# Kernel tuning notes

Hardware: AMD Instinct MI355X
Metric: run time of the kernel (lower is better)

## Reference

```python
import jax, jax.numpy as jnp
import numpy as np

RATIOS = (2, 2, 2)
IN_SIZE = 512
DATA_SIZE = 2
NOISE_BANDS = 5
TARGET_SIZE = int(np.prod(RATIOS))  # 8


def conv1d(x, w, b, stride):
    # cc.get_padding(3, stride, mode='centered'): total pad = 3 - stride = 1 -> (left, right) = (0, 1)
    y = jax.lax.conv_general_dilated(
        x, w, window_strides=(stride,), padding=[(0, 1)],
        dimension_numbers=('NCH', 'OIH', 'NCH'))
    return y + b[None, :, None]


def mod_sigmoid(x):
    return 2.0 * jax.nn.sigmoid(x) ** 2.3 + 1e-7


def amp_to_impulse_response(amp, target_size):
    # amp: [..., noise_bands] real, treated as complex spectrum with zero imag
    ir = jnp.fft.irfft(amp)                      # [..., 2*(nb-1)]
    fs = ir.shape[-1]
    ir = jnp.roll(ir, fs // 2, axis=-1)
    n = jnp.arange(fs, dtype=ir.dtype)
    win = 0.5 * (1.0 - jnp.cos(2.0 * jnp.pi * n / fs))  # periodic hann (torch default)
    ir = ir * win
    pad = int(target_size) - fs                   # 0 for our config
    ir = jnp.pad(ir, [(0, 0)] * (ir.ndim - 1) + [(0, pad)])
    return jnp.roll(ir, -(fs // 2), axis=-1)


def fft_convolve(signal, kernel):
    n = signal.shape[-1]
    pad_cfg = [(0, 0)] * (signal.ndim - 1)
    s = jnp.pad(signal, pad_cfg + [(0, n)])
    k = jnp.pad(kernel, pad_cfg + [(n, 0)])
    out = jnp.fft.irfft(jnp.fft.rfft(s) * jnp.fft.rfft(k))
    return out[..., out.shape[-1] // 2:]


def setup_inputs() -> dict:
    key = jax.random.key(0)
    ks = jax.random.split(key, 8)
    B, T = 16, 4096
    c_out = DATA_SIZE * NOISE_BANDS
    x = jax.random.normal(ks[0], (B, IN_SIZE, T), dtype=jnp.float32)
    noise = jax.random.uniform(ks[1], (B, T // TARGET_SIZE, DATA_SIZE, TARGET_SIZE), dtype=jnp.float32)
    w1 = jax.random.normal(ks[2], (IN_SIZE, IN_SIZE, 3), dtype=jnp.float32) * 0.03
    b1 = jnp.zeros((IN_SIZE,), dtype=jnp.float32)
    w2 = jax.random.normal(ks[3], (IN_SIZE, IN_SIZE, 3), dtype=jnp.float32) * 0.03
    b2 = jnp.zeros((IN_SIZE,), dtype=jnp.float32)
    w3 = jax.random.normal(ks[4], (c_out, IN_SIZE, 3), dtype=jnp.float32) * 0.03
    b3 = jnp.zeros((c_out,), dtype=jnp.float32)
    return {"x": x, "noise": noise, "w1": w1, "b1": b1, "w2": w2, "b2": b2, "w3": w3, "b3": b3}


def reference(x, noise, w1, b1, w2, b2, w3, b3):
    h = conv1d(x, w1, b1, RATIOS[0])
    h = jax.nn.leaky_relu(h, 0.2)
    h = conv1d(h, w2, b2, RATIOS[1])
    h = jax.nn.leaky_relu(h, 0.2)
    h = conv1d(h, w3, b3, RATIOS[2])            # [B, data_size*nb, T']
    amp = mod_sigmoid(h - 5.0)
    amp = jnp.transpose(amp, (0, 2, 1))          # [B, T', data_size*nb]
    B, Tp = amp.shape[0], amp.shape[1]
    amp = amp.reshape(B, Tp, DATA_SIZE, -1)      # [B, T', data_size, nb]
    ir = amp_to_impulse_response(amp, TARGET_SIZE)  # [B, T', data_size, target]
    nz = noise * 2.0 - 1.0                        # torch.rand_like(ir)*2-1
    out = fft_convolve(nz, ir)                    # [B, T', data_size, target]
    out = jnp.transpose(out, (0, 2, 1, 3))        # [B, data_size, T', target]
    return out.reshape(B, DATA_SIZE, -1)          # [B, data_size, T'*target]
```

## Files before the change

kernel.cpp:

```cpp
#include <hip/hip_runtime.h>
#include <math.h>


typedef __attribute__((ext_vector_type(8)))  short bf16x8;
typedef __attribute__((ext_vector_type(16))) float f32x16;

__device__ __forceinline__ unsigned short f2bf_rne(float f) {
    unsigned int u = __float_as_uint(f);
    unsigned int r = u + 0x7fff + ((u >> 16) & 1);
    return (unsigned short)(r >> 16);
}
__device__ __forceinline__ float bf2f(unsigned short h) {
    return __uint_as_float(((unsigned int)h) << 16);
}
__device__ __forceinline__ void gload_lds16(const void* g, void* l) {
    __builtin_amdgcn_global_load_lds(
        (const __attribute__((address_space(1))) unsigned int*)g,
        (__attribute__((address_space(3))) unsigned int*)l, 16, 0, 0);
}
__device__ __forceinline__ int swz1(int r) {
    return ((r >> 1) ^ (r >> 4)) & 7;
}

__global__ void prep_all(const float* __restrict__ W1, const float* __restrict__ W2,
                         short* __restrict__ Wf1, short* __restrict__ Wf2,
                         char* __restrict__ h1p, char* __restrict__ h2t)
{
    const int bid = blockIdx.x;
    const int tid = threadIdx.x;
    if (bid < 1536) {
        const float* W = (bid < 768) ? W1 : W2;
        short* Wf = (bid < 768) ? Wf1 : Wf2;
        int gid = ((bid < 768) ? bid : bid - 768) * 256 + tid;
        int f = gid >> 6, l = gid & 63;
        int ks = f & 1, hl = (f >> 1) & 1;
        int k  = (f >> 2) % 3;
        int rem = (f >> 2) / 3;
        int cob = rem & 15, cb = rem >> 4;
        int co  = cob * 32 + (l & 31);
        int ci0 = cb * 32 + ks * 16 + (l >> 5) * 8;
        bf16x8 o;
#pragma unroll
        for (int j = 0; j < 8; ++j) {
            float v = W[((size_t)co * 512 + ci0 + j) * 3 + k];
            unsigned short hi = f2bf_rne(v);
            o[j] = hl ? (short)f2bf_rne(v - bf2f(hi)) : (short)hi;
        }
        *(bf16x8*)((char*)Wf + (size_t)f * 1024 + l * 16) = o;
    } else {
        int id = (bid - 1536) * 256 + tid;
        if (id < 16384) {
            int b = id >> 10, w = id & 1023;
            *(float*)(h1p + ((size_t)b * 2080 + 2048) * 2048 + (size_t)w * 4) = 0.f;
        } else {
            int id2 = id - 16384;
            int b = id2 >> 10, w = id2 & 1023;
            *(float*)(h2t + ((size_t)b * 1026 + 1024) * 2048 + (size_t)w * 4) = 0.f;
        }
    }
}

__global__ __launch_bounds__(256, 2) void conv1_fused(
    const float* __restrict__ X, const short* __restrict__ Wf,
    const float* __restrict__ Bias, char* __restrict__ Out)
{
    __shared__ char AB[2][16512];

    const int tid = threadIdx.x;
    const int l   = tid & 63;
    const int wid = tid >> 6;
    const int tl0 = l & 31;
    const int lh  = l >> 5;

    int p = blockIdx.x;
    int chunk = p >> 5, slot = p & 31;
    int gl = slot & 15, c = slot >> 4;
    int g = chunk * 16 + gl;
    int zb = g >> 5, y = g & 31;

    const int bt0 = y * 64;
    const int r0  = 2 * bt0;
    const float* Xb = X + (size_t)zb * 512 * 4096;

    const int rg   = tid & 15;
    const int cip  = tid >> 4;
    const int ci   = 2 * cip;
    const int u_hi = ci >> 3;
    const int u_lo = 4 + u_hi;
    const int coff = (ci & 7) * 2;

    f32x16 acc[2][2];
#pragma unroll
    for (int tp = 0; tp < 2; ++tp)
#pragma unroll
        for (int cp = 0; cp < 2; ++cp) acc[tp][cp] = (f32x16)(0.0f);

    const int cbase = c * 8 + wid * 2;

    float4 fx0, fx1, fx2, fx3;
    float  fextra = 0.f;

    auto issue_loads = [&](int cb) {
        const float* s0 = Xb + (size_t)(cb * 32 + 2 * cip) * 4096 + r0 + rg * 8;
        fx0 = *(const float4*)(s0);
        fx1 = *(const float4*)(s0 + 4);
        fx2 = *(const float4*)(s0 + 4096);
        fx3 = *(const float4*)(s0 + 4100);
        if (tid < 32) {
            int rr = r0 + 128;
            fextra = (rr < 4096) ? Xb[(size_t)(cb * 32 + tid) * 4096 + rr] : 0.f;
        }
    };

    auto write_k = [&](char* buf, int k, float a, float b) {
        int r  = rg * 8 + k;
        int sw = swz1(r);
        unsigned int ua = __float_as_uint(a);
        unsigned int ub = __float_as_uint(b);
        float ha = __uint_as_float(ua & 0xffff0000u);
        float hb = __uint_as_float(ub & 0xffff0000u);
        unsigned short la = f2bf_rne(a - ha);
        unsigned short lb = f2bf_rne(b - hb);
        *(unsigned int*)(buf + r * 128 + ((u_hi ^ sw) << 4) + coff) =
            (ua >> 16) | (ub & 0xffff0000u);
        *(unsigned int*)(buf + r * 128 + ((u_lo ^ sw) << 4) + coff) =
            (unsigned int)la | ((unsigned int)lb << 16);
    };
    auto write_lo = [&](char* buf) {
        write_k(buf, 0, fx0.x, fx2.x);
        write_k(buf, 1, fx0.y, fx2.y);
        write_k(buf, 2, fx0.z, fx2.z);
        write_k(buf, 3, fx0.w, fx2.w);
    };
    auto write_hi = [&](char* buf) {
        write_k(buf, 4, fx1.x, fx3.x);
        write_k(buf, 5, fx1.y, fx3.y);
        write_k(buf, 6, fx1.z, fx3.z);
        write_k(buf, 7, fx1.w, fx3.w);
        if (tid < 32) {
            int sw = swz1(128);
            unsigned int ue = __float_as_uint(fextra);
            float he = __uint_as_float(ue & 0xffff0000u);
            unsigned short lo = f2bf_rne(fextra - he);
            int uh = (tid >> 3) ^ sw;
            int ul = (4 + (tid >> 3)) ^ sw;
            *(unsigned short*)(buf + 128 * 128 + (uh << 4) + (tid & 7) * 2) =
                (unsigned short)(ue >> 16);
            *(unsigned short*)(buf + 128 * 128 + (ul << 4) + (tid & 7) * 2) = lo;
        }
    };

    auto wptr = [&](int cb_, int cp, int tap, int ks, int hl) -> const char* {
        size_t f0 = ((((size_t)(cb_ * 16 + cbase + cp) * 3 + tap) * 2 + hl) * 2 + ks);
        return (const char*)Wf + f0 * 1024 + (size_t)l * 16;
    };

    issue_loads(0);
    write_lo(AB[0]);
    write_hi(AB[0]);
    __syncthreads();

    for (int cb = 0; cb < 16; ++cb) {
        const char* Ab = AB[cb & 1];
        char* Wb = (char*)AB[(cb + 1) & 1];

        bf16x8 bbA[12];
#pragma unroll
        for (int ph = 0; ph < 3; ++ph)
#pragma unroll
            for (int cp = 0; cp < 2; ++cp)
#pragma unroll
                for (int hl = 0; hl < 2; ++hl)
                    bbA[ph * 4 + cp * 2 + hl] =
                        *(const bf16x8*)wptr(cb, cp, ph >> 1, ph & 1, hl);
        if (cb < 15) issue_loads(cb + 1);

        __builtin_amdgcn_s_setprio(1);
#pragma unroll
        for (int ph = 0; ph < 3; ++ph) {
            const int tap = ph >> 1, ks = ph & 1;
            bf16x8 a0[2], a1[2];
#pragma unroll
            for (int tp = 0; tp < 2; ++tp) {
                int rl = 2 * (tp * 32 + tl0) + tap;
                int sw = swz1(rl);
                int qb = ks * 2 + lh;
                a0[tp] = *(const bf16x8*)(Ab + rl * 128 + ((qb ^ sw) << 4));
                a1[tp] = *(const bf16x8*)(Ab + rl * 128 + (((qb + 4) ^ sw) << 4));
            }
#pragma unroll
            for (int tp = 0; tp < 2; ++tp)
#pragma unroll
                for (int cp = 0; cp < 2; ++cp) {
                    acc[tp][cp] = __builtin_amdgcn_mfma_f32_32x32x16_bf16(
                        a0[tp], bbA[ph * 4 + cp * 2 + 0], acc[tp][cp], 0, 0, 0);
                    acc[tp][cp] = __builtin_amdgcn_mfma_f32_32x32x16_bf16(
                        a0[tp], bbA[ph * 4 + cp * 2 + 1], acc[tp][cp], 0, 0, 0);
                    acc[tp][cp] = __builtin_amdgcn_mfma_f32_32x32x16_bf16(
                        a1[tp], bbA[ph * 4 + cp * 2 + 0], acc[tp][cp], 0, 0, 0);
                }
        }
        __builtin_amdgcn_s_setprio(0);

        bf16x8 bbB[12];
#pragma unroll
        for (int ph = 3; ph < 6; ++ph)
#pragma unroll
            for (int cp = 0; cp < 2; ++cp)
#pragma unroll
                for (int hl = 0; hl < 2; ++hl)
                    bbB[(ph - 3) * 4 + cp * 2 + hl] =
                        *(const bf16x8*)wptr(cb, cp, ph >> 1, ph & 1, hl);

        if (cb < 15) write_lo(Wb);

        __builtin_amdgcn_s_setprio(1);
#pragma unroll
        for (int ph = 3; ph < 6; ++ph) {
            const int tap = ph >> 1, ks = ph & 1;
            bf16x8 a0[2], a1[2];
#pragma unroll
            for (int tp = 0; tp < 2; ++tp) {
                int rl = 2 * (tp * 32 + tl0) + tap;
                int sw = swz1(rl);
                int qb = ks * 2 + lh;
                a0[tp] = *(const bf16x8*)(Ab + rl * 128 + ((qb ^ sw) << 4));
                a1[tp] = *(const bf16x8*)(Ab + rl * 128 + (((qb + 4) ^ sw) << 4));
            }
#pragma unroll
            for (int tp = 0; tp < 2; ++tp)
#pragma unroll
                for (int cp = 0; cp < 2; ++cp) {
                    acc[tp][cp] = __builtin_amdgcn_mfma_f32_32x32x16_bf16(
                        a0[tp], bbB[(ph - 3) * 4 + cp * 2 + 0], acc[tp][cp], 0, 0, 0);
                    acc[tp][cp] = __builtin_amdgcn_mfma_f32_32x32x16_bf16(
                        a0[tp], bbB[(ph - 3) * 4 + cp * 2 + 1], acc[tp][cp], 0, 0, 0);
                    acc[tp][cp] = __builtin_amdgcn_mfma_f32_32x32x16_bf16(
                        a1[tp], bbB[(ph - 3) * 4 + cp * 2 + 0], acc[tp][cp], 0, 0, 0);
                }
        }
        __builtin_amdgcn_s_setprio(0);

        if (cb < 15) write_hi(Wb);
        __syncthreads();
    }

    const size_t outB = (size_t)zb * 2080 * 2048;
    const int colb = c * 256 + wid * 64 + tl0;
#pragma unroll
    for (int cp = 0; cp < 2; ++cp) {
        int co = colb + cp * 32;
        float bv = Bias[co];
#pragma unroll
        for (int tp = 0; tp < 2; ++tp) {
            int trow = bt0 + tp * 32 + 4 * lh;
#pragma unroll
            for (int r = 0; r < 16; ++r) {
                int row = trow + (r & 3) + 8 * (r >> 2);
                float v = acc[tp][cp][r] + bv;
                v = v < 0.f ? 0.2f * v : v;
                char* po = Out + outB + (size_t)row * 2048;
                unsigned int uv = __float_as_uint(v);
                float hf = __uint_as_float(uv & 0xffff0000u);
                *(unsigned short*)(po + co * 2) = (unsigned short)(uv >> 16);
                *(unsigned short*)(po + 1024 + co * 2) = f2bf_rne(v - hf);
            }
        }
    }
}

#define CONV_UNITS 1032

__global__ __launch_bounds__(256, 2) void conv_mfma(
    const char* __restrict__ Xp, const short* __restrict__ Wf,
    const float* __restrict__ Bias, char* __restrict__ Out,
    int rowsX, int rowsO, int Yt, int mode)
{
    __shared__ char AB[2][16512];

    const int tid = threadIdx.x;
    const int l   = tid & 63;
    const int wid = tid >> 6;
    const int tl0 = l & 31;
    const int lh  = l >> 5;

    int p = blockIdx.x;
    int chunk = p >> 5, slot = p & 31;
    int gl = slot & 15, c = slot >> 4;
    int g = chunk * 16 + gl;
    int zb = g / Yt, y = g - zb * Yt;

    const int bt0 = y * 64;
    const int r0  = 2 * bt0;
    const char* Xb = Xp + (size_t)zb * (size_t)rowsX * 2048;

    f32x16 acc[2][2];
#pragma unroll
    for (int tp = 0; tp < 2; ++tp)
#pragma unroll
        for (int cp = 0; cp < 2; ++cp) acc[tp][cp] = (f32x16)(0.0f);

    const int cbase = c * 8 + wid * 2;

    auto stage = [&](char* buf, int cb) {
#pragma unroll
        for (int i = 0; i < 5; ++i) {
            int u = i * 256 + tid;
            if (u < CONV_UNITS) {
                int r = u >> 3, ul = u & 7;
                int us = ul ^ ((r >> 1) & 7);
                const char* gp = Xb + (size_t)(r0 + r) * 2048
                               + (us >> 2) * 1024 + cb * 64 + (us & 3) * 16;
                gload_lds16(gp, buf + ((size_t)(i * 256 + wid * 64)) * 16);
            }
        }
    };

    stage(AB[0], 0);
    __syncthreads();

    for (int cb = 0; cb < 16; ++cb) {
        if (cb < 15) stage(AB[(cb + 1) & 1], cb + 1);
        const char* Ab = AB[cb & 1];
#pragma unroll
        for (int ph = 0; ph < 6; ++ph) {
            const int tap = ph >> 1, ks = ph & 1;
            bf16x8 a[2][2], bb[2][2];
#pragma unroll
            for (int tp = 0; tp < 2; ++tp) {
                int rl = 2 * (tp * 32 + tl0) + tap;
                int sw = (rl >> 1) & 7;
                int qb = ks * 2 + lh;
                a[0][tp] = *(const bf16x8*)(Ab + rl * 128 + ((qb ^ sw) << 4));
                a[1][tp] = *(const bf16x8*)(Ab + rl * 128 + (((qb + 4) ^ sw) << 4));
            }
#pragma unroll
            for (int cp = 0; cp < 2; ++cp) {
                size_t f0 = ((((size_t)(cb * 16 + cbase + cp) * 3 + tap) * 2 + 0) * 2 + ks);
                const char* wp = (const char*)Wf + f0 * 1024 + l * 16;
                bb[0][cp] = *(const bf16x8*)(wp);
                bb[1][cp] = *(const bf16x8*)(wp + 2048);
            }
#pragma unroll
            for (int tp = 0; tp < 2; ++tp)
#pragma unroll
                for (int cp = 0; cp < 2; ++cp) {
                    acc[tp][cp] = __builtin_amdgcn_mfma_f32_32x32x16_bf16(
                        a[0][tp], bb[0][cp], acc[tp][cp], 0, 0, 0);
                    acc[tp][cp] = __builtin_amdgcn_mfma_f32_32x32x16_bf16(
                        a[0][tp], bb[1][cp], acc[tp][cp], 0, 0, 0);
                    acc[tp][cp] = __builtin_amdgcn_mfma_f32_32x32x16_bf16(
                        a[1][tp], bb[0][cp], acc[tp][cp], 0, 0, 0);
                }
        }
        __syncthreads();
    }

    const size_t outB = (size_t)zb * (size_t)rowsO * 2048;
    const int colb = c * 256 + wid * 64 + tl0;
#pragma unroll
    for (int cp = 0; cp < 2; ++cp) {
        int co = colb + cp * 32;
        float bv = Bias[co];
#pragma unroll
        for (int tp = 0; tp < 2; ++tp) {
            int trow = bt0 + tp * 32 + 4 * lh;
#pragma unroll
            for (int r = 0; r < 16; ++r) {
                int row = trow + (r & 3) + 8 * (r >> 2);
                float v = acc[tp][cp][r] + bv;
                v = v < 0.f ? 0.2f * v : v;
                char* po = Out + outB + (size_t)row * 2048;
                if (mode == 0) {
                    unsigned short hi = f2bf_rne(v);
                    unsigned short lo = f2bf_rne(v - bf2f(hi));
                    *(unsigned short*)(po + co * 2) = hi;
                    *(unsigned short*)(po + 1024 + co * 2) = lo;
                } else {
                    *(float*)(po + (size_t)co * 4) = v;
                }
            }
        }
    }
}

__global__ __launch_bounds__(256) void conv3_tmaj(
    const float* __restrict__ H2, const float* __restrict__ W3,
    const float* __restrict__ B3, const float* __restrict__ Noise,
    float* __restrict__ Out)
{
    __shared__ float W3s[1536][10];
    __shared__ float Xe[32][40];
    __shared__ float Xo[32][40];
    __shared__ float hs[32][12];

    const int b   = blockIdx.y;
    const int t0  = blockIdx.x * 32;
    const int tid = threadIdx.x;
    const int t   = tid & 31;
    const int gch = tid >> 5;

    for (int idx = tid; idx < 15360; idx += 256) {
        int co = idx / 1536;
        int r  = idx - co * 1536;
        W3s[r][co] = W3[idx];
    }

    float acc3[2] = {0.f, 0.f};
    const float* Hb = H2 + (size_t)b * 1026 * 512;

    for (int c0 = 0; c0 < 512; c0 += 32) {
        __syncthreads();
        for (int idx = tid; idx < 33 * 32; idx += 256) {
            int pp = idx >> 5, ci = idx & 31;
            Xe[ci][pp] = Hb[(size_t)(2 * t0 + 2 * pp) * 512 + c0 + ci];
            Xo[ci][pp] = Hb[(size_t)(2 * t0 + 2 * pp + 1) * 512 + c0 + ci];
        }
        __syncthreads();

        for (int ci = 0; ci < 32; ++ci) {
            float xe0 = Xe[ci][t];
            float xo0 = Xo[ci][t];
            float xe1 = Xe[ci][t + 1];
            int r = (c0 + ci) * 3;
#pragma unroll
            for (int m = 0; m < 2; ++m) {
                int cc = gch + m * 8;
                if (cc < 10) {
                    acc3[m] = fmaf(W3s[r][cc], xe0,
                              fmaf(W3s[r + 1][cc], xo0,
                              fmaf(W3s[r + 2][cc], xe1, acc3[m])));
                }
            }
        }
    }

#pragma unroll
    for (int m = 0; m < 2; ++m) {
        int cc = gch + m * 8;
        if (cc < 10) hs[t][cc] = acc3[m] + B3[cc];
    }
    __syncthreads();

    if (tid < 64) {
        const int tt = tid & 31;
        const int d  = tid >> 5;

        float A[5];
#pragma unroll
        for (int j = 0; j < 5; ++j) {
            float h = hs[tt][d * 5 + j] - 5.f;
            float s = 1.f / (1.f + expf(-h));
            A[j] = 2.f * powf(s, 2.3f) + 1e-7f;
        }

        const float SQ = 0.70710678118654752f;
        const float c1[8] = {1.f, SQ, 0.f, -SQ, -1.f, -SQ, 0.f, SQ};
        const float c2[8] = {1.f, 0.f, -1.f, 0.f, 1.f, 0.f, -1.f, 0.f};
        const float c3[8] = {1.f, -SQ, 0.f, SQ, -1.f, SQ, 0.f, -SQ};
        const float c4[8] = {1.f, -1.f, 1.f, -1.f, 1.f, -1.f, 1.f, -1.f};
        const float wsh[8] = {1.f, 0.85355339059327376f, 0.5f, 0.14644660940672624f,
                              0.f, 0.14644660940672624f, 0.5f, 0.85355339059327376f};

        float ir[8];
#pragma unroll
        for (int n = 0; n < 8; ++n) {
            float v = A[0] + 2.f * (A[1] * c1[n] + A[2] * c2[n] + A[3] * c3[n])
                    + A[4] * c4[n];
            ir[n] = 0.125f * v * wsh[n];
        }

        const float* npi = Noise + (size_t)b * 8192 + (size_t)(t0 + tt) * 16 + d * 8;
        float nz[8];
#pragma unroll
        for (int j = 0; j < 8; ++j) nz[j] = 2.f * npi[j] - 1.f;

        float* op = Out + (size_t)b * 8192 + (size_t)d * 4096 + (size_t)(t0 + tt) * 8;
#pragma unroll
        for (int o = 0; o < 8; ++o) {
            float s = 0.f;
#pragma unroll
            for (int j = 0; j <= o; ++j) s += nz[j] * ir[o - j];
            op[o] = s;
        }
    }
}

#define BCO 64
#define BT  128
#define KC  16

__global__ __launch_bounds__(256, 2) void conv_s2_kernel(
    const float* __restrict__ X, const float* __restrict__ W,
    const float* __restrict__ Bias, float* __restrict__ Y,
    int Cin, int Tin, int Cout, int Tout, int leaky)
{
    __shared__ float Xe[KC][132];
    __shared__ float Xo[KC][132];
    __shared__ float Wk[KC * 3][68];

    const int b   = blockIdx.z;
    const int co0 = blockIdx.y * BCO;
    const int t0  = blockIdx.x * BT;
    const int tid = threadIdx.x;
    const int ty  = tid & 15;
    const int tx  = tid >> 4;

    const float* Xb = X + (size_t)b * Cin * Tin;

    float acc[4][8];
#pragma unroll
    for (int i = 0; i < 4; ++i)
#pragma unroll
        for (int j = 0; j < 8; ++j) acc[i][j] = 0.f;

    for (int c0 = 0; c0 < Cin; c0 += KC) {
        __syncthreads();
        for (int idx = tid; idx < KC * 130; idx += 256) {
            int ci = idx / 130;
            int pp = idx - ci * 130;
            int gt = 2 * t0 + 2 * pp;
            const float* src = Xb + (size_t)(c0 + ci) * Tin;
            float e, o;
            if (gt + 1 < Tin) {
                float2 v = *(const float2*)(src + gt);
                e = v.x; o = v.y;
            } else {
                e = (gt < Tin) ? src[gt] : 0.f;
                o = 0.f;
            }
            Xe[ci][pp] = e;
            Xo[ci][pp] = o;
        }
        {
            const float* Wc = W + (size_t)co0 * Cin * 3 + (size_t)c0 * 3;
            for (int idx = tid; idx < BCO * (KC * 3); idx += 256) {
                int co = idx / 48;
                int r  = idx - co * 48;
                Wk[r][co] = Wc[(size_t)co * Cin * 3 + r];
            }
        }
        __syncthreads();

#pragma unroll
        for (int ci = 0; ci < KC; ++ci) {
            float4 xe0 = *(const float4*)&Xe[ci][tx * 8];
            float4 xe1 = *(const float4*)&Xe[ci][tx * 8 + 4];
            float  xe8 = Xe[ci][tx * 8 + 8];
            float4 xo0 = *(const float4*)&Xo[ci][tx * 8];
            float4 xo1 = *(const float4*)&Xo[ci][tx * 8 + 4];
            float4 w0  = *(const float4*)&Wk[ci * 3 + 0][ty * 4];
            float4 w1  = *(const float4*)&Wk[ci * 3 + 1][ty * 4];
            float4 w2  = *(const float4*)&Wk[ci * 3 + 2][ty * 4];
            float xe[9] = {xe0.x, xe0.y, xe0.z, xe0.w, xe1.x, xe1.y, xe1.z, xe1.w, xe8};
            float xo[8] = {xo0.x, xo0.y, xo0.z, xo0.w, xo1.x, xo1.y, xo1.z, xo1.w};
            float wa[3][4] = {{w0.x, w0.y, w0.z, w0.w},
                              {w1.x, w1.y, w1.z, w1.w},
                              {w2.x, w2.y, w2.z, w2.w}};
#pragma unroll
            for (int i = 0; i < 4; ++i)
#pragma unroll
                for (int j = 0; j < 8; ++j)
                    acc[i][j] = fmaf(wa[0][i], xe[j],
                                fmaf(wa[1][i], xo[j],
                                fmaf(wa[2][i], xe[j + 1], acc[i][j])));
        }
    }

    float* Yb = Y + (size_t)b * Cout * Tout;
#pragma unroll
    for (int i = 0; i < 4; ++i) {
        int   co = co0 + ty * 4 + i;
        float bv = Bias[co];
        float ov[8];
#pragma unroll
        for (int j = 0; j < 8; ++j) {
            float v = acc[i][j] + bv;
            ov[j] = (leaky && v < 0.f) ? 0.2f * v : v;
        }
        float* dst = Yb + (size_t)co * Tout + t0 + tx * 8;
        *(float4*)dst       = make_float4(ov[0], ov[1], ov[2], ov[3]);
        *(float4*)(dst + 4) = make_float4(ov[4], ov[5], ov[6], ov[7]);
    }
}

__global__ __launch_bounds__(256) void conv3_cmaj(
    const float* __restrict__ H2, const float* __restrict__ W3,
    const float* __restrict__ B3, const float* __restrict__ Noise,
    float* __restrict__ Out)
{
    __shared__ float W3s[1536][10];
    __shared__ float Xe[32][40];
    __shared__ float Xo[32][40];
    __shared__ float hs[32][12];

    const int b   = blockIdx.y;
    const int t0  = blockIdx.x * 32;
    const int tid = threadIdx.x;
    const int t   = tid & 31;
    const int gch = tid >> 5;

    for (int idx = tid; idx < 15360; idx += 256) {
        int co = idx / 1536;
        int r  = idx - co * 1536;
        W3s[r][co] = W3[idx];
    }

    float acc3[2] = {0.f, 0.f};
    const float* Hb = H2 + (size_t)b * 512 * 1024;

    for (int c0 = 0; c0 < 512; c0 += 32) {
        __syncthreads();
        for (int idx = tid; idx < 32 * 33; idx += 256) {
            int ci = idx / 33;
            int pp = idx - ci * 33;
            int gt = 2 * t0 + 2 * pp;
            const float* src = Hb + (size_t)(c0 + ci) * 1024;
            float e, o;
            if (gt + 1 < 1024) {
                float2 v = *(const float2*)(src + gt);
                e = v.x; o = v.y;
            } else {
                e = (gt < 1024) ? src[gt] : 0.f;
                o = 0.f;
            }
            Xe[ci][pp] = e;
            Xo[ci][pp] = o;
        }
        __syncthreads();

        for (int ci = 0; ci < 32; ++ci) {
            float xe0 = Xe[ci][t];
            float xo0 = Xo[ci][t];
            float xe1 = Xe[ci][t + 1];
            int r = (c0 + ci) * 3;
#pragma unroll
            for (int m = 0; m < 2; ++m) {
                int cc = gch + m * 8;
                if (cc < 10)
                    acc3[m] = fmaf(W3s[r][cc], xe0,
                              fmaf(W3s[r + 1][cc], xo0,
                              fmaf(W3s[r + 2][cc], xe1, acc3[m])));
            }
        }
    }

#pragma unroll
    for (int m = 0; m < 2; ++m) {
        int cc = gch + m * 8;
        if (cc < 10) hs[t][cc] = acc3[m] + B3[cc];
    }
    __syncthreads();

    if (tid < 64) {
        const int tt = tid & 31;
        const int d  = tid >> 5;
        float A[5];
#pragma unroll
        for (int j = 0; j < 5; ++j) {
            float h = hs[tt][d * 5 + j] - 5.f;
            float s = 1.f / (1.f + expf(-h));
            A[j] = 2.f * powf(s, 2.3f) + 1e-7f;
        }
        const float SQ = 0.70710678118654752f;
        const float c1[8] = {1.f, SQ, 0.f, -SQ, -1.f, -SQ, 0.f, SQ};
        const float c2[8] = {1.f, 0.f, -1.f, 0.f, 1.f, 0.f, -1.f, 0.f};
        const float c3[8] = {1.f, -SQ, 0.f, SQ, -1.f, SQ, 0.f, -SQ};
        const float c4[8] = {1.f, -1.f, 1.f, -1.f, 1.f, -1.f, 1.f, -1.f};
        const float wsh[8] = {1.f, 0.85355339059327376f, 0.5f, 0.14644660940672624f,
                              0.f, 0.14644660940672624f, 0.5f, 0.85355339059327376f};
        float ir[8];
#pragma unroll
        for (int n = 0; n < 8; ++n) {
            float v = A[0] + 2.f * (A[1] * c1[n] + A[2] * c2[n] + A[3] * c3[n])
                    + A[4] * c4[n];
            ir[n] = 0.125f * v * wsh[n];
        }
        const float* npi = Noise + (size_t)b * 8192 + (size_t)(t0 + tt) * 16 + d * 8;
        float nz[8];
#pragma unroll
        for (int j = 0; j < 8; ++j) nz[j] = 2.f * npi[j] - 1.f;
        float* op = Out + (size_t)b * 8192 + (size_t)d * 4096 + (size_t)(t0 + tt) * 8;
#pragma unroll
        for (int o = 0; o < 8; ++o) {
            float s = 0.f;
#pragma unroll
            for (int j = 0; j <= o; ++j) s += nz[j] * ir[o - j];
            op[o] = s;
        }
    }
}

extern "C" void kernel_launch(void* const* d_in, const int* in_sizes, int n_in,
                              void* d_out, int out_size, void* d_ws, size_t ws_size,
                              hipStream_t stream) {
    const float* x     = (const float*)d_in[0];
    const float* noise = (const float*)d_in[1];
    const float* w1    = (const float*)d_in[2];
    const float* b1    = (const float*)d_in[3];
    const float* w2    = (const float*)d_in[4];
    const float* b2    = (const float*)d_in[5];
    const float* w3    = (const float*)d_in[6];
    const float* b3    = (const float*)d_in[7];
    float* out = (float*)d_out;

    const size_t H1P_BYTES = (size_t)16 * 2080 * 2048;
    const size_t H2T_BYTES = (size_t)16 * 1026 * 512 * 4;
    const size_t WF_BYTES  = (size_t)512 * 512 * 3 * 2 * 2;
    const size_t NEED = H1P_BYTES + H2T_BYTES + 2 * WF_BYTES;

    if (ws_size >= NEED) {
        char*  h1p = (char*)d_ws;
        char*  h2t = h1p + H1P_BYTES;
        short* Wf1 = (short*)(h2t + H2T_BYTES);
        short* Wf2 = (short*)((char*)Wf1 + WF_BYTES);

        prep_all<<<1664, 256, 0, stream>>>(w1, w2, Wf1, Wf2, h1p, h2t);
        conv1_fused<<<1024, 256, 0, stream>>>(x, Wf1, b1, h1p);
        conv_mfma<<<512, 256, 0, stream>>>(h1p, Wf2, b2, h2t, 2080, 1026, 16, 1);
        conv3_tmaj<<<dim3(16, 16), 256, 0, stream>>>((const float*)h2t, w3, b3, noise, out);
    } else {
        float* h1 = (float*)d_ws;
        float* h2 = h1 + (size_t)16 * 512 * 2048;
        dim3 blk(256);
        conv_s2_kernel<<<dim3(2048 / BT, 512 / BCO, 16), blk, 0, stream>>>(
            x, w1, b1, h1, 512, 4096, 512, 2048, 1);
        conv_s2_kernel<<<dim3(1024 / BT, 512 / BCO, 16), blk, 0, stream>>>(
            h1, w2, b2, h2, 512, 2048, 512, 1024, 1);
        conv3_cmaj<<<dim3(16, 16), blk, 0, stream>>>(h2, w3, b3, noise, out);
    }
}
```

Before: 315.4 us.

## Split conv MFMA tiles across 8 waves per block instead of 4

Both conv1_fused and conv_mfma now run 512 threads per block. Each wave owns one 32-row time tile and two channel tiles, where before each of 4 waves owned two time tiles. Staging loads are redistributed over the larger block, and conv1's split A/B weight prefetch with setprio phases is replaced by a simpler per-phase load loop. The intent is more waves for latency hiding with fewer accumulator registers per wave. The cost is dropping the explicit weight-prefetch overlap, and each wave now reloads the weight fragments that one wave previously reused across two time tiles.

After: 350.4 us. 11.1% more time.

```diff
diff --git a/kernel.cpp b/kernel.cpp
--- a/kernel.cpp
+++ b/kernel.cpp
@@ -60,7 +60,7 @@
     }
 }
 
-__global__ __launch_bounds__(256, 2) void conv1_fused(
+__global__ __launch_bounds__(512, 2) void conv1_fused(
     const float* __restrict__ X, const short* __restrict__ Wf,
     const float* __restrict__ Bias, char* __restrict__ Out)
 {
@@ -69,6 +69,8 @@
     const int tid = threadIdx.x;
     const int l   = tid & 63;
     const int wid = tid >> 6;
+    const int cw  = wid & 3;
+    const int tw  = wid >> 2;
     const int tl0 = l & 31;
     const int lh  = l >> 5;
 
@@ -82,30 +84,26 @@
     const int r0  = 2 * bt0;
     const float* Xb = X + (size_t)zb * 512 * 4096;
 
-    const int rg   = tid & 15;
-    const int cip  = tid >> 4;
+    const int rg   = tid & 31;
+    const int cip  = tid >> 5;
     const int ci   = 2 * cip;
     const int u_hi = ci >> 3;
     const int u_lo = 4 + u_hi;
     const int coff = (ci & 7) * 2;
 
-    f32x16 acc[2][2];
-#pragma unroll
-    for (int tp = 0; tp < 2; ++tp)
-#pragma unroll
-        for (int cp = 0; cp < 2; ++cp) acc[tp][cp] = (f32x16)(0.0f);
-
-    const int cbase = c * 8 + wid * 2;
-
-    float4 fx0, fx1, fx2, fx3;
+    f32x16 acc[2];
+    acc[0] = (f32x16)(0.0f);
+    acc[1] = (f32x16)(0.0f);
+
+    const int cbase = c * 8 + cw * 2;
+
+    float4 fx0, fx2;
     float  fextra = 0.f;
 
     auto issue_loads = [&](int cb) {
-        const float* s0 = Xb + (size_t)(cb * 32 + 2 * cip) * 4096 + r0 + rg * 8;
+        const float* s0 = Xb + (size_t)(cb * 32 + ci) * 4096 + r0 + rg * 4;
         fx0 = *(const float4*)(s0);
-        fx1 = *(const float4*)(s0 + 4);
         fx2 = *(const float4*)(s0 + 4096);
-        fx3 = *(const float4*)(s0 + 4100);
         if (tid < 32) {
             int rr = r0 + 128;
             fextra = (rr < 4096) ? Xb[(size_t)(cb * 32 + tid) * 4096 + rr] : 0.f;
@@ -113,7 +111,7 @@
     };
 
     auto write_k = [&](char* buf, int k, float a, float b) {
-        int r  = rg * 8 + k;
+        int r  = rg * 4 + k;
         int sw = swz1(r);
         unsigned int ua = __float_as_uint(a);
         unsigned int ub = __float_as_uint(b);
@@ -126,17 +124,11 @@
         *(unsigned int*)(buf + r * 128 + ((u_lo ^ sw) << 4) + coff) =
             (unsigned int)la | ((unsigned int)lb << 16);
     };
-    auto write_lo = [&](char* buf) {
+    auto write_tile = [&](char* buf) {
         write_k(buf, 0, fx0.x, fx2.x);
         write_k(buf, 1, fx0.y, fx2.y);
         write_k(buf, 2, fx0.z, fx2.z);
         write_k(buf, 3, fx0.w, fx2.w);
-    };
-    auto write_hi = [&](char* buf) {
-        write_k(buf, 4, fx1.x, fx3.x);
-        write_k(buf, 5, fx1.y, fx3.y);
-        write_k(buf, 6, fx1.z, fx3.z);
-        write_k(buf, 7, fx1.w, fx3.w);
         if (tid < 32) {
             int sw = swz1(128);
             unsigned int ue = __float_as_uint(fextra);
@@ -156,122 +148,67 @@
     };
 
     issue_loads(0);
-    write_lo(AB[0]);
-    write_hi(AB[0]);
+    write_tile(AB[0]);
     __syncthreads();
 
     for (int cb = 0; cb < 16; ++cb) {
+        if (cb < 15) issue_loads(cb + 1);
         const char* Ab = AB[cb & 1];
-        char* Wb = (char*)AB[(cb + 1) & 1];
-
-        bf16x8 bbA[12];
-#pragma unroll
-        for (int ph = 0; ph < 3; ++ph)
-#pragma unroll
-            for (int cp = 0; cp < 2; ++cp)
-#pragma unroll
-                for (int hl = 0; hl < 2; ++hl)
-                    bbA[ph * 4 + cp * 2 + hl] =
-                        *(const bf16x8*)wptr(cb, cp, ph >> 1, ph & 1, hl);
-        if (cb < 15) issue_loads(cb + 1);
-
-        __builtin_amdgcn_s_setprio(1);
-#pragma unroll
-        for (int ph = 0; ph < 3; ++ph) {
+#pragma unroll
+        for (int ph = 0; ph < 6; ++ph) {
             const int tap = ph >> 1, ks = ph & 1;
-            bf16x8 a0[2], a1[2];
-#pragma unroll
-            for (int tp = 0; tp < 2; ++tp) {
-                int rl = 2 * (tp * 32 + tl0) + tap;
+            bf16x8 a0, a1, bb[2][2];
+            {
+                int rl = 2 * (tw * 32 + tl0) + tap;
                 int sw = swz1(rl);
                 int qb = ks * 2 + lh;
-                a0[tp] = *(const bf16x8*)(Ab + rl * 128 + ((qb ^ sw) << 4));
-                a1[tp] = *(const bf16x8*)(Ab + rl * 128 + (((qb + 4) ^ sw) << 4));
-            }
-#pragma unroll
-            for (int tp = 0; tp < 2; ++tp)
-#pragma unroll
-                for (int cp = 0; cp < 2; ++cp) {
-                    acc[tp][cp] = __builtin_amdgcn_mfma_f32_32x32x16_bf16(
-                        a0[tp], bbA[ph * 4 + cp * 2 + 0], acc[tp][cp], 0, 0, 0);
-                    acc[tp][cp] = __builtin_amdgcn_mfma_f32_32x32x16_bf16(
-                        a0[tp], bbA[ph * 4 + cp * 2 + 1], acc[tp][cp], 0, 0, 0);
-                    acc[tp][cp] = __builtin_amdgcn_mfma_f32_32x32x16_bf16(
-                        a1[tp], bbA[ph * 4 + cp * 2 + 0], acc[tp][cp], 0, 0, 0);
-                }
-        }
-        __builtin_amdgcn_s_setprio(0);
-
-        bf16x8 bbB[12];
-#pragma unroll
-        for (int ph = 3; ph < 6; ++ph)
-#pragma unroll
-            for (int cp = 0; cp < 2; ++cp)
-#pragma unroll
-                for (int hl = 0; hl < 2; ++hl)
-                    bbB[(ph - 3) * 4 + cp * 2 + hl] =
-                        *(const bf16x8*)wptr(cb, cp, ph >> 1, ph & 1, hl);
-
-        if (cb < 15) write_lo(Wb);
-
-        __builtin_amdgcn_s_setprio(1);
-#pragma unroll
-        for (int ph = 3; ph < 6; ++ph) {
-            const int tap = ph >> 1, ks = ph & 1;
-            bf16x8 a0[2], a1[2];
-#pragma unroll
-            for (int tp = 0; tp < 2; ++tp) {
-                int rl = 2 * (tp * 32 + tl0) + tap;
-                int sw = swz1(rl);
-                int qb = ks * 2 + lh;
-                a0[tp] = *(const bf16x8*)(Ab + rl * 128 + ((qb ^ sw) << 4));
-                a1[tp] = *(const bf16x8*)(Ab + rl * 128 + (((qb + 4) ^ sw) << 4));
-            }
-#pragma unroll
-            for (int tp = 0; tp < 2; ++tp)
-#pragma unroll
-                for (int cp = 0; cp < 2; ++cp) {
-                    acc[tp][cp] = __builtin_amdgcn_mfma_f32_32x32x16_bf16(
-                        a0[tp], bbB[(ph - 3) * 4 + cp * 2 + 0], acc[tp][cp], 0, 0, 0);
-                    acc[tp][cp] = __builtin_amdgcn_mfma_f32_32x32x16_bf16(
-                        a0[tp], bbB[(ph - 3) * 4 + cp * 2 + 1], acc[tp][cp], 0, 0, 0);
-                    acc[tp][cp] = __builtin_amdgcn_mfma_f32_32x32x16_bf16(
-                        a1[tp], bbB[(ph - 3) * 4 + cp * 2 + 0], acc[tp][cp], 0, 0, 0);
-                }
-        }
-        __builtin_amdgcn_s_setprio(0);
-
-        if (cb < 15) write_hi(Wb);
+                a0 = *(const bf16x8*)(Ab + rl * 128 + ((qb ^ sw) << 4));
+                a1 = *(const bf16x8*)(Ab + rl * 128 + (((qb + 4) ^ sw) << 4));
+            }
+#pragma unroll
+            for (int cp = 0; cp < 2; ++cp) {
+                const char* wp = wptr(cb, cp, tap, ks, 0);
+                bb[0][cp] = *(const bf16x8*)(wp);
+                bb[1][cp] = *(const bf16x8*)(wp + 2048);
+            }
+#pragma unroll
+            for (int cp = 0; cp < 2; ++cp) {
+                acc[cp] = __builtin_amdgcn_mfma_f32_32x32x16_bf16(
+                    a0, bb[0][cp], acc[cp], 0, 0, 0);
+                acc[cp] = __builtin_amdgcn_mfma_f32_32x32x16_bf16(
+                    a0, bb[1][cp], acc[cp], 0, 0, 0);
+                acc[cp] = __builtin_amdgcn_mfma_f32_32x32x16_bf16(
+                    a1, bb[0][cp], acc[cp], 0, 0, 0);
+            }
+        }
+        if (cb < 15) write_tile((char*)AB[(cb + 1) & 1]);
         __syncthreads();
     }
 
     const size_t outB = (size_t)zb * 2080 * 2048;
-    const int colb = c * 256 + wid * 64 + tl0;
+    const int colb = c * 256 + cw * 64 + tl0;
 #pragma unroll
     for (int cp = 0; cp < 2; ++cp) {
         int co = colb + cp * 32;
         float bv = Bias[co];
-#pragma unroll
-        for (int tp = 0; tp < 2; ++tp) {
-            int trow = bt0 + tp * 32 + 4 * lh;
-#pragma unroll
-            for (int r = 0; r < 16; ++r) {
-                int row = trow + (r & 3) + 8 * (r >> 2);
-                float v = acc[tp][cp][r] + bv;
-                v = v < 0.f ? 0.2f * v : v;
-                char* po = Out + outB + (size_t)row * 2048;
-                unsigned int uv = __float_as_uint(v);
-                float hf = __uint_as_float(uv & 0xffff0000u);
-                *(unsigned short*)(po + co * 2) = (unsigned short)(uv >> 16);
-                *(unsigned short*)(po + 1024 + co * 2) = f2bf_rne(v - hf);
-            }
+        int trow = bt0 + tw * 32 + 4 * lh;
+#pragma unroll
+        for (int r = 0; r < 16; ++r) {
+            int row = trow + (r & 3) + 8 * (r >> 2);
+            float v = acc[cp][r] + bv;
+            v = v < 0.f ? 0.2f * v : v;
+            char* po = Out + outB + (size_t)row * 2048;
+            unsigned int uv = __float_as_uint(v);
+            float hf = __uint_as_float(uv & 0xffff0000u);
+            *(unsigned short*)(po + co * 2) = (unsigned short)(uv >> 16);
+            *(unsigned short*)(po + 1024 + co * 2) = f2bf_rne(v - hf);
         }
     }
 }
 
 #define CONV_UNITS 1032
 
-__global__ __launch_bounds__(256, 2) void conv_mfma(
+__global__ __launch_bounds__(512, 2) void conv_mfma(
     const char* __restrict__ Xp, const short* __restrict__ Wf,
     const float* __restrict__ Bias, char* __restrict__ Out,
     int rowsX, int rowsO, int Yt, int mode)
@@ -281,6 +218,8 @@
     const int tid = threadIdx.x;
     const int l   = tid & 63;
     const int wid = tid >> 6;
+    const int cw  = wid & 3;
+    const int tw  = wid >> 2;
     const int tl0 = l & 31;
     const int lh  = l >> 5;
 
@@ -294,24 +233,22 @@
     const int r0  = 2 * bt0;
     const char* Xb = Xp + (size_t)zb * (size_t)rowsX * 2048;
 
-    f32x16 acc[2][2];
-#pragma unroll
-    for (int tp = 0; tp < 2; ++tp)
-#pragma unroll
-        for (int cp = 0; cp < 2; ++cp) acc[tp][cp] = (f32x16)(0.0f);
-
-    const int cbase = c * 8 + wid * 2;
+    f32x16 acc[2];
+    acc[0] = (f32x16)(0.0f);
+    acc[1] = (f32x16)(0.0f);
+
+    const int cbase = c * 8 + cw * 2;
 
     auto stage = [&](char* buf, int cb) {
 #pragma unroll
-        for (int i = 0; i < 5; ++i) {
-            int u = i * 256 + tid;
+        for (int i = 0; i < 3; ++i) {
+            int u = i * 512 + tid;
             if (u < CONV_UNITS) {
                 int r = u >> 3, ul = u & 7;
                 int us = ul ^ ((r >> 1) & 7);
                 const char* gp = Xb + (size_t)(r0 + r) * 2048
                                + (us >> 2) * 1024 + cb * 64 + (us & 3) * 16;
-                gload_lds16(gp, buf + ((size_t)(i * 256 + wid * 64)) * 16);
+                gload_lds16(gp, buf + ((size_t)(i * 512 + wid * 64)) * 16);
             }
         }
     };
@@ -325,14 +262,13 @@
 #pragma unroll
         for (int ph = 0; ph < 6; ++ph) {
             const int tap = ph >> 1, ks = ph & 1;
-            bf16x8 a[2][2], bb[2][2];
-#pragma unroll
-            for (int tp = 0; tp < 2; ++tp) {
-                int rl = 2 * (tp * 32 + tl0) + tap;
+            bf16x8 a0, a1, bb[2][2];
+            {
+                int rl = 2 * (tw * 32 + tl0) + tap;
                 int sw = (rl >> 1) & 7;
                 int qb = ks * 2 + lh;
-                a[0][tp] = *(const bf16x8*)(Ab + rl * 128 + ((qb ^ sw) << 4));
-                a[1][tp] = *(const bf16x8*)(Ab + rl * 128 + (((qb + 4) ^ sw) << 4));
+                a0 = *(const bf16x8*)(Ab + rl * 128 + ((qb ^ sw) << 4));
+                a1 = *(const bf16x8*)(Ab + rl * 128 + (((qb + 4) ^ sw) << 4));
             }
 #pragma unroll
             for (int cp = 0; cp < 2; ++cp) {
@@ -342,43 +278,38 @@
                 bb[1][cp] = *(const bf16x8*)(wp + 2048);
             }
 #pragma unroll
-            for (int tp = 0; tp < 2; ++tp)
-#pragma unroll
-                for (int cp = 0; cp < 2; ++cp) {
-                    acc[tp][cp] = __builtin_amdgcn_mfma_f32_32x32x16_bf16(
-                        a[0][tp], bb[0][cp], acc[tp][cp], 0, 0, 0);
-                    acc[tp][cp] = __builtin_amdgcn_mfma_f32_32x32x16_bf16(
-                        a[0][tp], bb[1][cp], acc[tp][cp], 0, 0, 0);
-                    acc[tp][cp] = __builtin_amdgcn_mfma_f32_32x32x16_bf16(
-                        a[1][tp], bb[0][cp], acc[tp][cp], 0, 0, 0);
-                }
+            for (int cp = 0; cp < 2; ++cp) {
+                acc[cp] = __builtin_amdgcn_mfma_f32_32x32x16_bf16(
+                    a0, bb[0][cp], acc[cp], 0, 0, 0);
+                acc[cp] = __builtin_amdgcn_mfma_f32_32x32x16_bf16(
+                    a0, bb[1][cp], acc[cp], 0, 0, 0);
+                acc[cp] = __builtin_amdgcn_mfma_f32_32x32x16_bf16(
+                    a1, bb[0][cp], acc[cp], 0, 0, 0);
+            }
         }
         __syncthreads();
     }
 
     const size_t outB = (size_t)zb * (size_t)rowsO * 2048;
-    const int colb = c * 256 + wid * 64 + tl0;
+    const int colb = c * 256 + cw * 64 + tl0;
 #pragma unroll
     for (int cp = 0; cp < 2; ++cp) {
         int co = colb + cp * 32;
         float bv = Bias[co];
-#pragma unroll
-        for (int tp = 0; tp < 2; ++tp) {
-            int trow = bt0 + tp * 32 + 4 * lh;
-#pragma unroll
-            for (int r = 0; r < 16; ++r) {
-                int row = trow + (r & 3) + 8 * (r >> 2);
-                float v = acc[tp][cp][r] + bv;
-                v = v < 0.f ? 0.2f * v : v;
-                char* po = Out + outB + (size_t)row * 2048;
-                if (mode == 0) {
-                    unsigned short hi = f2bf_rne(v);
-                    unsigned short lo = f2bf_rne(v - bf2f(hi));
-                    *(unsigned short*)(po + co * 2) = hi;
-                    *(unsigned short*)(po + 1024 + co * 2) = lo;
-                } else {
-                    *(float*)(po + (size_t)co * 4) = v;
-                }
+        int trow = bt0 + tw * 32 + 4 * lh;
+#pragma unroll
+        for (int r = 0; r < 16; ++r) {
+            int row = trow + (r & 3) + 8 * (r >> 2);
+            float v = acc[cp][r] + bv;
+            v = v < 0.f ? 0.2f * v : v;
+            char* po = Out + outB + (size_t)row * 2048;
+            if (mode == 0) {
+                unsigned short hi = f2bf_rne(v);
+                unsigned short lo = f2bf_rne(v - bf2f(hi));
+                *(unsigned short*)(po + co * 2) = hi;
+                *(unsigned short*)(po + 1024 + co * 2) = lo;
+            } else {
+                *(float*)(po + (size_t)co * 4) = v;
             }
         }
     }
@@ -716,8 +647,8 @@
         short* Wf2 = (short*)((char*)Wf1 + WF_BYTES);
 
         prep_all<<<1664, 256, 0, stream>>>(w1, w2, Wf1, Wf2, h1p, h2t);
-        conv1_fused<<<1024, 256, 0, stream>>>(x, Wf1, b1, h1p);
-        conv_mfma<<<512, 256, 0, stream>>>(h1p, Wf2, b2, h2t, 2080, 1026, 16, 1);
+        conv1_fused<<<1024, 512, 0, stream>>>(x, Wf1, b1, h1p);
+        conv_mfma<<<512, 512, 0, stream>>>(h1p, Wf2, b2, h2t, 2080, 1026, 16, 1);
         conv3_tmaj<<<dim3(16, 16), 256, 0, stream>>>((const float*)h2t, w3, b3, noise, out);
     } else {
         float* h1 = (float*)d_ws;
```
